# Optimization experiments

Measured on AMD Instinct MI355X. Metric: run time of the kernel, lower is better.

The kernel has to match this reference:

```python
import jax, jax.numpy as jnp
import numpy as np

H, W = 256, 832
B = 2
SEARCH_W, SEARCH_H = 7, 3
SPARSITY_RAD = 2
SENSE_RANGE = 10
PIX_W = 20.0          # pixel_distance_weight
ALPHA_W = 0.7         # alpha_distance_weight
MULLINE_W = 15.0      # pixel_mulline_distance_weight
ALPHA_PAD = 0.6       # alpha_padding
INF = 1e9


def _sorted_offsets(span_x, span_y):
    xs, ys = np.meshgrid(span_x, span_y)
    xs = xs.flatten(); ys = ys.flatten()
    order = np.argsort(xs ** 2 + ys ** 2, kind='stable')
    return xs[order].astype(np.int32), ys[order].astype(np.int32)


def setup_inputs() -> dict:
    key = jax.random.key(0)
    k1, k2 = jax.random.split(key)
    src = (jax.random.uniform(k1, (B, 1, H, W)) < 0.02).astype(jnp.float32)
    dst = (jax.random.uniform(k2, (B, 1, H, W)) < 0.02).astype(jnp.float32)
    xx, yy = _sorted_offsets(np.arange(-SEARCH_W, SEARCH_W + 1), np.arange(-SEARCH_H, SEARCH_H + 1))
    sxs, sys_ = np.meshgrid(np.arange(-SPARSITY_RAD, SPARSITY_RAD + 1), np.arange(-SPARSITY_RAD, SPARSITY_RAD + 1))
    sxx = sxs.flatten().astype(np.int32); syy = sys_.flatten().astype(np.int32)
    cxx, cyy = _sorted_offsets(np.arange(-SENSE_RANGE, SENSE_RANGE + 1), np.arange(-SENSE_RANGE, SENSE_RANGE + 1))
    return {"binMapsrc": src, "binMapdst": dst,
            "xx": jnp.asarray(xx), "yy": jnp.asarray(yy),
            "sxx": jnp.asarray(sxx), "syy": jnp.asarray(syy),
            "cxx": jnp.asarray(cxx), "cyy": jnp.asarray(cyy)}


def _orientation(m):
    # local edge orientation from a 3x3 box-blurred map
    b = sum(jnp.roll(jnp.roll(m, di, 0), dj, 1) for di in (-1, 0, 1) for dj in (-1, 0, 1))
    gy, gx = jnp.gradient(b)
    return jnp.arctan2(gy, gx)


def _morph_single(src, dst, xx, yy, sxx, syy, cxx, cyy):
    gy, gx = jnp.meshgrid(jnp.arange(H, dtype=jnp.int32), jnp.arange(W, dtype=jnp.int32), indexing='ij')

    def gather(offy, offx, arr, fill):
        ii = gy[None] + offy[:, None, None]          # [K,H,W]
        jj = gx[None] + offx[:, None, None]
        inb = (ii >= 0) & (ii < H) & (jj >= 0) & (jj < W)
        vals = arr[jnp.clip(ii, 0, H - 1), jnp.clip(jj, 0, W - 1)]
        return jnp.where(inb, vals, fill)

    src_e = src > 0.5
    # --- sparsify source edge points: keep min-linear-index edge in each sparsity window ---
    lin = jnp.where(src_e, (gy * W + gx).astype(jnp.float32), INF)
    keep = src_e & (lin == gather(syy, sxx, lin, INF).min(0))
    # --- windowed correspondence search with distance + orientation scoring ---
    theta_s = _orientation(src)
    theta_d = _orientation(dst)
    hit = gather(yy, xx, dst, 0.0) > 0.5             # [K,H,W]
    ang = 1.0 - jnp.cos(theta_s[None] - gather(yy, xx, theta_d, 0.0))
    dist = jnp.sqrt((xx * xx + yy * yy).astype(jnp.float32))
    score = jnp.where(hit, PIX_W * dist[:, None, None] + MULLINE_W * ALPHA_W * ang, INF)
    kbest = jnp.argmin(score, axis=0)                # [H,W]
    active = keep & (score.min(0) < 0.5 * INF)
    dispx = jnp.where(active, xx[kbest].astype(jnp.float32), 0.0)
    dispy = jnp.where(active, yy[kbest].astype(jnp.float32), 0.0)
    # --- diffuse sparse displacements over the sense window (scan keeps memory small) ---
    R = SENSE_RANGE
    pad = lambda a: jnp.pad(a, ((R, R), (R, R)))
    pdx, pdy, pm = pad(dispx), pad(dispy), pad(active.astype(jnp.float32))
    wk = jnp.exp(-jnp.sqrt((cxx * cxx + cyy * cyy).astype(jnp.float32)) / (0.5 * R))

    def body(carry, inp):
        nx, ny, den = carry
        dy_, dx_, w = inp
        sl = lambda a: jax.lax.dynamic_slice(a, (R + dy_, R + dx_), (H, W))
        return (nx + w * sl(pdx), ny + w * sl(pdy), den + w * sl(pm)), None

    zeros = jnp.zeros((H, W), jnp.float32)
    (nx, ny, den), _ = jax.lax.scan(body, (zeros, zeros, zeros), (cyy, cxx, wk))
    mdx = ALPHA_PAD * nx / (den + 1e-6)
    mdy = ALPHA_PAD * ny / (den + 1e-6)
    morphedx = gx.astype(jnp.float32) + mdx
    morphedy = gy.astype(jnp.float32) + mdy
    return jnp.stack([morphedx, morphedy], 0)        # [2,H,W]


def reference(binMapsrc, binMapdst, xx, yy, sxx, syy, cxx, cyy):
    f = lambda s, d: _morph_single(s, d, xx, yy, sxx, syy, cxx, cyy)
    return jax.vmap(f)(binMapsrc[:, 0], binMapdst[:, 0])  # [B,2,H,W]
```

## Files before the change

kernel.cpp:

```cpp
#include <hip/hip_runtime.h>
#include <math.h>

#define BB 2
#define HH 256
#define WW 832
#define HWIMG (HH * WW)
#define BHW (BB * HWIMG)

#define TXN 26
#define TYN 8
#define NTILES (BB * TXN * TYN)
#define CAP 512
#define LDSK 128

__device__ inline float theta_at(const float* __restrict__ m, int i, int j) {
    int ri[5], cj[5];
#pragma unroll
    for (int t = 0; t < 5; ++t) {
        int r = i + t - 2; r = (r < 0) ? r + HH : (r >= HH ? r - HH : r);
        int c = j + t - 2; c = (c < 0) ? c + WW : (c >= WW ? c - WW : c);
        ri[t] = r * WW; cj[t] = c;
    }
    float S[5][5];
#pragma unroll
    for (int a = 0; a < 5; ++a)
#pragma unroll
        for (int c = 0; c < 5; ++c)
            S[a][c] = m[ri[a] + cj[c]];
    float ct[5], cm[5], cb[5];
#pragma unroll
    for (int c = 0; c < 5; ++c) {
        ct[c] = S[0][c] + S[1][c] + S[2][c];
        cm[c] = S[1][c] + S[2][c] + S[3][c];
        cb[c] = S[2][c] + S[3][c] + S[4][c];
    }
    float Bm = ct[1] + ct[2] + ct[3];
    float Bp = cb[1] + cb[2] + cb[3];
    float Bl = cm[0] + cm[1] + cm[2];
    float Br = cm[2] + cm[3] + cm[4];
    float Bc = cm[1] + cm[2] + cm[3];
    float gy = (i == 0) ? (Bp - Bc) : (i == HH - 1) ? (Bc - Bm) : 0.5f * (Bp - Bm);
    float gx = (j == 0) ? (Br - Bc) : (j == WW - 1) ? (Bc - Bl) : 0.5f * (Br - Bl);
    return atan2f(gy, gx);
}

__global__ void fused_kernel(const float* __restrict__ src, const float* __restrict__ dst,
                             const int* __restrict__ xx, const int* __restrict__ yy, int K,
                             int* __restrict__ counts, int* __restrict__ entries) {
    __shared__ int kox[128], koy[128];
    __shared__ float kd[128];
    __shared__ int recs[LDSK];
    __shared__ float tss[LDSK];
    __shared__ int nkeep;

    int tid = threadIdx.x;
    if (tid == 0) nkeep = 0;
    for (int t = tid; t < K; t += 256) {
        int ox = xx[t], oy = yy[t];
        kox[t] = ox; koy[t] = oy;
        kd[t] = 20.0f * sqrtf((float)(ox * ox + oy * oy));
    }
    __syncthreads();

    int idx = blockIdx.x * 256 + tid;
    int j = idx % WW;
    int r = idx / WW;
    int i = r % HH;
    int b = r / HH;
    const float* sb = src + b * HWIMG;
    const float* db = dst + b * HWIMG;

    if (sb[i * WW + j] > 0.5f) {
        float m = 0.f;
#pragma unroll
        for (int p = 0; p < 12; ++p) {
            int di = (p < 5) ? -2 : (p < 10 ? -1 : 0);
            int dj = (p < 5) ? (p - 2) : (p < 10 ? (p - 7) : (p - 12));
            int ii = i + di, jj = j + dj;
            bool inb = (ii >= 0) && (jj >= 0) && (jj < WW);
            float v = sb[inb ? (ii * WW + jj) : 0];
            m = fmaxf(m, inb ? v : 0.f);
        }
        if (m <= 0.5f) {
            float ts = theta_at(sb, i, j);
            int pos = atomicAdd(&nkeep, 1);
            if (pos < LDSK) {
                recs[pos] = j | (i << 10) | (b << 18);
                tss[pos] = ts;
            }
        }
    }
    __syncthreads();

    int nk = (nkeep < LDSK) ? nkeep : LDSK;
    int lane = tid & 63;
    int wv = tid >> 6;
    for (int w = wv; w < nk; w += 4) {
        int rec = recs[w];
        float ts = tss[w];
        int kj = rec & 1023;
        int ki = (rec >> 10) & 255;
        int kb = rec >> 18;
        const float* d = dst + kb * HWIMG;

        float best = 1e9f;
        int bk = 1 << 20;
#pragma unroll
        for (int rr = 0; rr < 2; ++rr) {
            int k = lane + rr * 64;
            if (k < K) {
                int ii = ki + koy[k], jj = kj + kox[k];
                if (ii >= 0 && ii < HH && jj >= 0 && jj < WW && d[ii * WW + jj] > 0.5f) {
                    float td = theta_at(d, ii, jj);
                    float sc = kd[k] + 10.5f * (1.0f - cosf(ts - td));
                    if (sc < best || (sc == best && k < bk)) { best = sc; bk = k; }
                }
            }
        }
#pragma unroll
        for (int off = 32; off >= 1; off >>= 1) {
            float ob = __shfl_down(best, off, 64);
            int ok = __shfl_down(bk, off, 64);
            if (ob < best || (ob == best && ok < bk)) { best = ob; bk = ok; }
        }
        if (lane == 0 && best < 5e8f) {
            int dx = kox[bk], dy = koy[bk];
            int packed = kj | (ki << 10) | ((dx + 7) << 18) | ((dy + 3) << 22);
            int tx0 = max(kj - 10, 0) >> 5, tx1 = min(kj + 10, WW - 1) >> 5;
            int ty0 = max(ki - 10, 0) >> 5, ty1 = min(ki + 10, HH - 1) >> 5;
            for (int ty = ty0; ty <= ty1; ++ty)
                for (int tx = tx0; tx <= tx1; ++tx) {
                    int tile = (kb * TYN + ty) * TXN + tx;
                    int pos = atomicAdd(&counts[tile], 1);
                    if (pos < CAP) entries[tile * CAP + pos] = packed;
                }
        }
    }
}

__global__ void diffuse_kernel(const int* __restrict__ counts, const int* __restrict__ entries,
                               float* __restrict__ out) {
    __shared__ float wt[441];
    __shared__ float4 ent[CAP];
    int tid = threadIdx.y * 32 + threadIdx.x;
    for (int t = tid; t < 441; t += 256) {
        int dy = t / 21 - 10;
        int dx = t % 21 - 10;
        wt[t] = expf(-sqrtf((float)(dx * dx + dy * dy)) / 5.0f);
    }
    int tx = blockIdx.x, ty = blockIdx.y, b = blockIdx.z;
    int tile = (b * TYN + ty) * TXN + tx;
    int cnt = counts[tile];
    if (cnt > CAP) cnt = CAP;
    const int* e = entries + tile * CAP;
    for (int t = tid; t < cnt; t += 256) {
        int p = e[t];
        ent[t] = make_float4((float)(p & 1023), (float)((p >> 10) & 255),
                             (float)(((p >> 18) & 15) - 7), (float)(((p >> 22) & 7) - 3));
    }
    __syncthreads();

    int j = tx * 32 + threadIdx.x;
    int i0 = ty * 32 + threadIdx.y * 4;
    float nx0 = 0, ny0 = 0, de0 = 0;
    float nx1 = 0, ny1 = 0, de1 = 0;
    float nx2 = 0, ny2 = 0, de2 = 0;
    float nx3 = 0, ny3 = 0, de3 = 0;

    for (int c = 0; c < cnt; ++c) {
        float4 E = ent[c];
        int dj = (int)E.x - j;
        if (dj < -10 || dj > 10) continue;
        int di = (int)E.y - i0;
        const float* wrow = &wt[dj + 10];
        if (di >= -10 && di <= 10) { float w = wrow[(di + 10) * 21]; de0 += w; nx0 += w * E.z; ny0 += w * E.w; }
        if (di >= -9  && di <= 11) { float w = wrow[(di + 9)  * 21]; de1 += w; nx1 += w * E.z; ny1 += w * E.w; }
        if (di >= -8  && di <= 12) { float w = wrow[(di + 8)  * 21]; de2 += w; nx2 += w * E.z; ny2 += w * E.w; }
        if (di >= -7  && di <= 13) { float w = wrow[(di + 7)  * 21]; de3 += w; nx3 += w * E.z; ny3 += w * E.w; }
    }

    int obase = b * 2 * HWIMG;
    float inv;
    inv = 0.6f / (de0 + 1e-6f);
    out[obase + (i0 + 0) * WW + j] = (float)j + nx0 * inv;
    out[obase + HWIMG + (i0 + 0) * WW + j] = (float)(i0 + 0) + ny0 * inv;
    inv = 0.6f / (de1 + 1e-6f);
    out[obase + (i0 + 1) * WW + j] = (float)j + nx1 * inv;
    out[obase + HWIMG + (i0 + 1) * WW + j] = (float)(i0 + 1) + ny1 * inv;
    inv = 0.6f / (de2 + 1e-6f);
    out[obase + (i0 + 2) * WW + j] = (float)j + nx2 * inv;
    out[obase + HWIMG + (i0 + 2) * WW + j] = (float)(i0 + 2) + ny2 * inv;
    inv = 0.6f / (de3 + 1e-6f);
    out[obase + (i0 + 3) * WW + j] = (float)j + nx3 * inv;
    out[obase + HWIMG + (i0 + 3) * WW + j] = (float)(i0 + 3) + ny3 * inv;
}

extern "C" void kernel_launch(void* const* d_in, const int* in_sizes, int n_in,
                              void* d_out, int out_size, void* d_ws, size_t ws_size,
                              hipStream_t stream) {
    const float* src = (const float*)d_in[0];
    const float* dst = (const float*)d_in[1];
    const int* xx = (const int*)d_in[2];
    const int* yy = (const int*)d_in[3];
    int K = in_sizes[2];

    int* counts  = (int*)d_ws;
    int* entries = counts + NTILES;
    float* out = (float*)d_out;

    hipMemsetAsync(counts, 0, NTILES * sizeof(int), stream);
    fused_kernel<<<dim3(BHW / 256), dim3(256), 0, stream>>>(
        src, dst, xx, yy, K, counts, entries);
    diffuse_kernel<<<dim3(TXN, TYN, BB), dim3(32, 8), 0, stream>>>(counts, entries, out);
}
```

Baseline: 110.7 us.

## Merge edge selection, matching and diffusion into one cooperative kernel

Replaces the memset and the two kernel launches with a single cooperative kernel of 416 blocks that uses grid-wide syncs between phases. Tile counts are zeroed inside the kernel, and each thread now scans four source pixels loaded as a float4, so the block count matches the diffusion tile count. This is meant to remove launch and memset overhead. In exchange it pays for two grid barriers, cuts the parallelism of the scan phase by four, and adds per-block serial work over its retained edge points.

New measurement: 220.0 us. 98.7% more time.

```diff
diff --git a/kernel.cpp b/kernel.cpp
--- a/kernel.cpp
+++ b/kernel.cpp
@@ -1,5 +1,8 @@
 #include <hip/hip_runtime.h>
+#include <hip/hip_cooperative_groups.h>
 #include <math.h>
+
+namespace cg = cooperative_groups;
 
 #define BB 2
 #define HH 256
@@ -44,155 +47,170 @@
     return atan2f(gy, gx);
 }
 
-__global__ void fused_kernel(const float* __restrict__ src, const float* __restrict__ dst,
-                             const int* __restrict__ xx, const int* __restrict__ yy, int K,
-                             int* __restrict__ counts, int* __restrict__ entries) {
+__global__ void mega_kernel(const float4* __restrict__ src4, const float* __restrict__ src,
+                            const float* __restrict__ dst,
+                            const int* __restrict__ xx, const int* __restrict__ yy, int K,
+                            int* __restrict__ counts, int* __restrict__ entries,
+                            float* __restrict__ out) {
     __shared__ int kox[128], koy[128];
     __shared__ float kd[128];
     __shared__ int recs[LDSK];
     __shared__ float tss[LDSK];
     __shared__ int nkeep;
-
+    __shared__ float wt[441];
+    __shared__ float4 ent[CAP];
+
+    cg::grid_group grid = cg::this_grid();
     int tid = threadIdx.x;
-    if (tid == 0) nkeep = 0;
+    int bid = blockIdx.x;
+
+    if (tid == 0) { nkeep = 0; counts[bid] = 0; }
     for (int t = tid; t < K; t += 256) {
         int ox = xx[t], oy = yy[t];
         kox[t] = ox; koy[t] = oy;
         kd[t] = 20.0f * sqrtf((float)(ox * ox + oy * oy));
     }
-    __syncthreads();
-
-    int idx = blockIdx.x * 256 + tid;
-    int j = idx % WW;
-    int r = idx / WW;
-    int i = r % HH;
-    int b = r / HH;
-    const float* sb = src + b * HWIMG;
-    const float* db = dst + b * HWIMG;
-
-    if (sb[i * WW + j] > 0.5f) {
-        float m = 0.f;
-#pragma unroll
-        for (int p = 0; p < 12; ++p) {
-            int di = (p < 5) ? -2 : (p < 10 ? -1 : 0);
-            int dj = (p < 5) ? (p - 2) : (p < 10 ? (p - 7) : (p - 12));
-            int ii = i + di, jj = j + dj;
-            bool inb = (ii >= 0) && (jj >= 0) && (jj < WW);
-            float v = sb[inb ? (ii * WW + jj) : 0];
-            m = fmaxf(m, inb ? v : 0.f);
-        }
-        if (m <= 0.5f) {
-            float ts = theta_at(sb, i, j);
-            int pos = atomicAdd(&nkeep, 1);
-            if (pos < LDSK) {
-                recs[pos] = j | (i << 10) | (b << 18);
-                tss[pos] = ts;
-            }
-        }
-    }
-    __syncthreads();
-
-    int nk = (nkeep < LDSK) ? nkeep : LDSK;
-    int lane = tid & 63;
-    int wv = tid >> 6;
-    for (int w = wv; w < nk; w += 4) {
-        int rec = recs[w];
-        float ts = tss[w];
-        int kj = rec & 1023;
-        int ki = (rec >> 10) & 255;
-        int kb = rec >> 18;
-        const float* d = dst + kb * HWIMG;
-
-        float best = 1e9f;
-        int bk = 1 << 20;
-#pragma unroll
-        for (int rr = 0; rr < 2; ++rr) {
-            int k = lane + rr * 64;
-            if (k < K) {
-                int ii = ki + koy[k], jj = kj + kox[k];
-                if (ii >= 0 && ii < HH && jj >= 0 && jj < WW && d[ii * WW + jj] > 0.5f) {
-                    float td = theta_at(d, ii, jj);
-                    float sc = kd[k] + 10.5f * (1.0f - cosf(ts - td));
-                    if (sc < best || (sc == best && k < bk)) { best = sc; bk = k; }
-                }
-            }
-        }
-#pragma unroll
-        for (int off = 32; off >= 1; off >>= 1) {
-            float ob = __shfl_down(best, off, 64);
-            int ok = __shfl_down(bk, off, 64);
-            if (ob < best || (ob == best && ok < bk)) { best = ob; bk = ok; }
-        }
-        if (lane == 0 && best < 5e8f) {
-            int dx = kox[bk], dy = koy[bk];
-            int packed = kj | (ki << 10) | ((dx + 7) << 18) | ((dy + 3) << 22);
-            int tx0 = max(kj - 10, 0) >> 5, tx1 = min(kj + 10, WW - 1) >> 5;
-            int ty0 = max(ki - 10, 0) >> 5, ty1 = min(ki + 10, HH - 1) >> 5;
-            for (int ty = ty0; ty <= ty1; ++ty)
-                for (int tx = tx0; tx <= tx1; ++tx) {
-                    int tile = (kb * TYN + ty) * TXN + tx;
-                    int pos = atomicAdd(&counts[tile], 1);
-                    if (pos < CAP) entries[tile * CAP + pos] = packed;
-                }
-        }
-    }
-}
-
-__global__ void diffuse_kernel(const int* __restrict__ counts, const int* __restrict__ entries,
-                               float* __restrict__ out) {
-    __shared__ float wt[441];
-    __shared__ float4 ent[CAP];
-    int tid = threadIdx.y * 32 + threadIdx.x;
     for (int t = tid; t < 441; t += 256) {
         int dy = t / 21 - 10;
         int dx = t % 21 - 10;
         wt[t] = expf(-sqrtf((float)(dx * dx + dy * dy)) / 5.0f);
     }
-    int tx = blockIdx.x, ty = blockIdx.y, b = blockIdx.z;
-    int tile = (b * TYN + ty) * TXN + tx;
-    int cnt = counts[tile];
-    if (cnt > CAP) cnt = CAP;
-    const int* e = entries + tile * CAP;
-    for (int t = tid; t < cnt; t += 256) {
-        int p = e[t];
-        ent[t] = make_float4((float)(p & 1023), (float)((p >> 10) & 255),
-                             (float)(((p >> 18) & 15) - 7), (float)(((p >> 22) & 7) - 3));
-    }
     __syncthreads();
 
-    int j = tx * 32 + threadIdx.x;
-    int i0 = ty * 32 + threadIdx.y * 4;
-    float nx0 = 0, ny0 = 0, de0 = 0;
-    float nx1 = 0, ny1 = 0, de1 = 0;
-    float nx2 = 0, ny2 = 0, de2 = 0;
-    float nx3 = 0, ny3 = 0, de3 = 0;
-
-    for (int c = 0; c < cnt; ++c) {
-        float4 E = ent[c];
-        int dj = (int)E.x - j;
-        if (dj < -10 || dj > 10) continue;
-        int di = (int)E.y - i0;
-        const float* wrow = &wt[dj + 10];
-        if (di >= -10 && di <= 10) { float w = wrow[(di + 10) * 21]; de0 += w; nx0 += w * E.z; ny0 += w * E.w; }
-        if (di >= -9  && di <= 11) { float w = wrow[(di + 9)  * 21]; de1 += w; nx1 += w * E.z; ny1 += w * E.w; }
-        if (di >= -8  && di <= 12) { float w = wrow[(di + 8)  * 21]; de2 += w; nx2 += w * E.z; ny2 += w * E.w; }
-        if (di >= -7  && di <= 13) { float w = wrow[(di + 7)  * 21]; de3 += w; nx3 += w * E.z; ny3 += w * E.w; }
-    }
-
-    int obase = b * 2 * HWIMG;
-    float inv;
-    inv = 0.6f / (de0 + 1e-6f);
-    out[obase + (i0 + 0) * WW + j] = (float)j + nx0 * inv;
-    out[obase + HWIMG + (i0 + 0) * WW + j] = (float)(i0 + 0) + ny0 * inv;
-    inv = 0.6f / (de1 + 1e-6f);
-    out[obase + (i0 + 1) * WW + j] = (float)j + nx1 * inv;
-    out[obase + HWIMG + (i0 + 1) * WW + j] = (float)(i0 + 1) + ny1 * inv;
-    inv = 0.6f / (de2 + 1e-6f);
-    out[obase + (i0 + 2) * WW + j] = (float)j + nx2 * inv;
-    out[obase + HWIMG + (i0 + 2) * WW + j] = (float)(i0 + 2) + ny2 * inv;
-    inv = 0.6f / (de3 + 1e-6f);
-    out[obase + (i0 + 3) * WW + j] = (float)j + nx3 * inv;
-    out[obase + HWIMG + (i0 + 3) * WW + j] = (float)(i0 + 3) + ny3 * inv;
+    {
+        int t4 = bid * 256 + tid;
+        float4 sv = src4[t4];
+        int p0 = t4 * 4;
+        int j0 = p0 % WW;
+        int r = p0 / WW;
+        int i = r % HH;
+        int b = r / HH;
+        const float* sb = src + b * HWIMG;
+        float svv[4] = {sv.x, sv.y, sv.z, sv.w};
+#pragma unroll
+        for (int q = 0; q < 4; ++q) {
+            if (svv[q] > 0.5f) {
+                int j = j0 + q;
+                float m = 0.f;
+#pragma unroll
+                for (int p = 0; p < 12; ++p) {
+                    int di = (p < 5) ? -2 : (p < 10 ? -1 : 0);
+                    int dj = (p < 5) ? (p - 2) : (p < 10 ? (p - 7) : (p - 12));
+                    int ii = i + di, jj = j + dj;
+                    bool inb = (ii >= 0) && (jj >= 0) && (jj < WW);
+                    float v = sb[inb ? (ii * WW + jj) : 0];
+                    m = fmaxf(m, inb ? v : 0.f);
+                }
+                if (m <= 0.5f) {
+                    float ts = theta_at(sb, i, j);
+                    int pos = atomicAdd(&nkeep, 1);
+                    if (pos < LDSK) {
+                        recs[pos] = j | (i << 10) | (b << 18);
+                        tss[pos] = ts;
+                    }
+                }
+            }
+        }
+    }
+    grid.sync();
+
+    {
+        int nk = (nkeep < LDSK) ? nkeep : LDSK;
+        int lane = tid & 63;
+        int wv = tid >> 6;
+        for (int w = wv; w < nk; w += 4) {
+            int rec = recs[w];
+            float ts = tss[w];
+            int kj = rec & 1023;
+            int ki = (rec >> 10) & 255;
+            int kb = rec >> 18;
+            const float* d = dst + kb * HWIMG;
+
+            float best = 1e9f;
+            int bk = 1 << 20;
+#pragma unroll
+            for (int rr = 0; rr < 2; ++rr) {
+                int k = lane + rr * 64;
+                if (k < K) {
+                    int ii = ki + koy[k], jj = kj + kox[k];
+                    if (ii >= 0 && ii < HH && jj >= 0 && jj < WW && d[ii * WW + jj] > 0.5f) {
+                        float td = theta_at(d, ii, jj);
+                        float sc = kd[k] + 10.5f * (1.0f - cosf(ts - td));
+                        if (sc < best || (sc == best && k < bk)) { best = sc; bk = k; }
+                    }
+                }
+            }
+#pragma unroll
+            for (int off = 32; off >= 1; off >>= 1) {
+                float ob = __shfl_down(best, off, 64);
+                int ok = __shfl_down(bk, off, 64);
+                if (ob < best || (ob == best && ok < bk)) { best = ob; bk = ok; }
+            }
+            if (lane == 0 && best < 5e8f) {
+                int dx = kox[bk], dy = koy[bk];
+                int packed = kj | (ki << 10) | ((dx + 7) << 18) | ((dy + 3) << 22);
+                int tx0 = max(kj - 10, 0) >> 5, tx1 = min(kj + 10, WW - 1) >> 5;
+                int ty0 = max(ki - 10, 0) >> 5, ty1 = min(ki + 10, HH - 1) >> 5;
+                for (int ty = ty0; ty <= ty1; ++ty)
+                    for (int tx = tx0; tx <= tx1; ++tx) {
+                        int tile = (kb * TYN + ty) * TXN + tx;
+                        int pos = atomicAdd(&counts[tile], 1);
+                        if (pos < CAP) entries[tile * CAP + pos] = packed;
+                    }
+            }
+        }
+    }
+    grid.sync();
+
+    {
+        int b = bid / (TYN * TXN);
+        int rem = bid % (TYN * TXN);
+        int ty = rem / TXN;
+        int tx = rem % TXN;
+        int cnt = counts[bid];
+        if (cnt > CAP) cnt = CAP;
+        const int* e = entries + bid * CAP;
+        for (int t = tid; t < cnt; t += 256) {
+            int p = e[t];
+            ent[t] = make_float4((float)(p & 1023), (float)((p >> 10) & 255),
+                                 (float)(((p >> 18) & 15) - 7), (float)(((p >> 22) & 7) - 3));
+        }
+        __syncthreads();
+
+        int j = tx * 32 + (tid & 31);
+        int i0 = ty * 32 + (tid >> 5) * 4;
+        float nx0 = 0, ny0 = 0, de0 = 0;
+        float nx1 = 0, ny1 = 0, de1 = 0;
+        float nx2 = 0, ny2 = 0, de2 = 0;
+        float nx3 = 0, ny3 = 0, de3 = 0;
+
+        for (int c = 0; c < cnt; ++c) {
+            float4 E = ent[c];
+            int dj = (int)E.x - j;
+            if (dj < -10 || dj > 10) continue;
+            int di = (int)E.y - i0;
+            const float* wrow = &wt[dj + 10];
+            if (di >= -10 && di <= 10) { float w = wrow[(di + 10) * 21]; de0 += w; nx0 += w * E.z; ny0 += w * E.w; }
+            if (di >= -9  && di <= 11) { float w = wrow[(di + 9)  * 21]; de1 += w; nx1 += w * E.z; ny1 += w * E.w; }
+            if (di >= -8  && di <= 12) { float w = wrow[(di + 8)  * 21]; de2 += w; nx2 += w * E.z; ny2 += w * E.w; }
+            if (di >= -7  && di <= 13) { float w = wrow[(di + 7)  * 21]; de3 += w; nx3 += w * E.z; ny3 += w * E.w; }
+        }
+
+        int obase = b * 2 * HWIMG;
+        float inv;
+        inv = 0.6f / (de0 + 1e-6f);
+        out[obase + (i0 + 0) * WW + j] = (float)j + nx0 * inv;
+        out[obase + HWIMG + (i0 + 0) * WW + j] = (float)(i0 + 0) + ny0 * inv;
+        inv = 0.6f / (de1 + 1e-6f);
+        out[obase + (i0 + 1) * WW + j] = (float)j + nx1 * inv;
+        out[obase + HWIMG + (i0 + 1) * WW + j] = (float)(i0 + 1) + ny1 * inv;
+        inv = 0.6f / (de2 + 1e-6f);
+        out[obase + (i0 + 2) * WW + j] = (float)j + nx2 * inv;
+        out[obase + HWIMG + (i0 + 2) * WW + j] = (float)(i0 + 2) + ny2 * inv;
+        inv = 0.6f / (de3 + 1e-6f);
+        out[obase + (i0 + 3) * WW + j] = (float)j + nx3 * inv;
+        out[obase + HWIMG + (i0 + 3) * WW + j] = (float)(i0 + 3) + ny3 * inv;
+    }
 }
 
 extern "C" void kernel_launch(void* const* d_in, const int* in_sizes, int n_in,
@@ -207,9 +225,10 @@
     int* counts  = (int*)d_ws;
     int* entries = counts + NTILES;
     float* out = (float*)d_out;
-
-    hipMemsetAsync(counts, 0, NTILES * sizeof(int), stream);
-    fused_kernel<<<dim3(BHW / 256), dim3(256), 0, stream>>>(
-        src, dst, xx, yy, K, counts, entries);
-    diffuse_kernel<<<dim3(TXN, TYN, BB), dim3(32, 8), 0, stream>>>(counts, entries, out);
+    const float4* src4 = (const float4*)src;
+
+    void* args[] = {(void*)&src4, (void*)&src, (void*)&dst, (void*)&xx, (void*)&yy,
+                    (void*)&K, (void*)&counts, (void*)&entries, (void*)&out};
+    hipLaunchCooperativeKernel((void*)mega_kernel, dim3(NTILES), dim3(256),
+                               args, 0, stream);
 }
```

## Fuse keypoint detection, matching and diffusion into one tile kernel with LDS halos

Applied to the files above, without the earlier changes.

Replaces the memset, the global keypoint/matching kernel and the diffusion kernel with a single per-tile kernel. Each 32x32 tile loads halo windows of the src and dst maps into LDS. It recomputes the sparse source keypoints for its 52x52 neighbourhood, matches them against dst in LDS, and diffuses the results directly. This removes the global atomics, the entry buffer round trip and two launches, at the cost of redundant keypoint and matching work in overlapping halos and larger LDS use.

After: 117.2 us. 1.06x slower.

```diff
diff --git a/kernel.cpp b/kernel.cpp
--- a/kernel.cpp
+++ b/kernel.cpp
@@ -5,28 +5,24 @@
 #define HH 256
 #define WW 832
 #define HWIMG (HH * WW)
-#define BHW (BB * HWIMG)
 
 #define TXN 26
 #define TYN 8
-#define NTILES (BB * TXN * TYN)
-#define CAP 512
-#define LDSK 128
-
-__device__ inline float theta_at(const float* __restrict__ m, int i, int j) {
-    int ri[5], cj[5];
-#pragma unroll
-    for (int t = 0; t < 5; ++t) {
-        int r = i + t - 2; r = (r < 0) ? r + HH : (r >= HH ? r - HH : r);
-        int c = j + t - 2; c = (c < 0) ? c + WW : (c >= WW ? c - WW : c);
-        ri[t] = r * WW; cj[t] = c;
-    }
+#define CAP 256
+
+#define SH 56
+#define SW 56
+#define DH 62
+#define DW 70
+
+__device__ inline float theta_lds(const float* a, int pitch, int ly, int lx,
+                                  int gi, int gj) {
     float S[5][5];
 #pragma unroll
-    for (int a = 0; a < 5; ++a)
+    for (int r = 0; r < 5; ++r)
 #pragma unroll
         for (int c = 0; c < 5; ++c)
-            S[a][c] = m[ri[a] + cj[c]];
+            S[r][c] = a[(ly + r - 2) * pitch + (lx + c - 2)];
     float ct[5], cm[5], cb[5];
 #pragma unroll
     for (int c = 0; c < 5; ++c) {
@@ -39,160 +35,159 @@
     float Bl = cm[0] + cm[1] + cm[2];
     float Br = cm[2] + cm[3] + cm[4];
     float Bc = cm[1] + cm[2] + cm[3];
-    float gy = (i == 0) ? (Bp - Bc) : (i == HH - 1) ? (Bc - Bm) : 0.5f * (Bp - Bm);
-    float gx = (j == 0) ? (Br - Bc) : (j == WW - 1) ? (Bc - Bl) : 0.5f * (Br - Bl);
+    float gy = (gi == 0) ? (Bp - Bc) : (gi == HH - 1) ? (Bc - Bm) : 0.5f * (Bp - Bm);
+    float gx = (gj == 0) ? (Br - Bc) : (gj == WW - 1) ? (Bc - Bl) : 0.5f * (Br - Bl);
     return atan2f(gy, gx);
 }
 
-__global__ void fused_kernel(const float* __restrict__ src, const float* __restrict__ dst,
-                             const int* __restrict__ xx, const int* __restrict__ yy, int K,
-                             int* __restrict__ counts, int* __restrict__ entries) {
+__global__ void __launch_bounds__(256, 2)
+bnmorph_kernel(const float* __restrict__ src, const float* __restrict__ dst,
+               const int* __restrict__ xx, const int* __restrict__ yy, int K,
+               float* __restrict__ out) {
+    __shared__ float srcW[SH * SW];
+    __shared__ float dstW[DH * DW];
+    __shared__ float wt[441];
     __shared__ int kox[128], koy[128];
     __shared__ float kd[128];
-    __shared__ int recs[LDSK];
-    __shared__ float tss[LDSK];
+    __shared__ float4 ent[CAP];
     __shared__ int nkeep;
 
     int tid = threadIdx.x;
+    int tx = blockIdx.x, ty = blockIdx.y, b = blockIdx.z;
+    int ti = ty * 32, tj = tx * 32;
+    const float* sb = src + b * HWIMG;
+    const float* db = dst + b * HWIMG;
+
     if (tid == 0) nkeep = 0;
     for (int t = tid; t < K; t += 256) {
         int ox = xx[t], oy = yy[t];
         kox[t] = ox; koy[t] = oy;
         kd[t] = 20.0f * sqrtf((float)(ox * ox + oy * oy));
     }
-    __syncthreads();
-
-    int idx = blockIdx.x * 256 + tid;
-    int j = idx % WW;
-    int r = idx / WW;
-    int i = r % HH;
-    int b = r / HH;
-    const float* sb = src + b * HWIMG;
-    const float* db = dst + b * HWIMG;
-
-    if (sb[i * WW + j] > 0.5f) {
-        float m = 0.f;
-#pragma unroll
-        for (int p = 0; p < 12; ++p) {
-            int di = (p < 5) ? -2 : (p < 10 ? -1 : 0);
-            int dj = (p < 5) ? (p - 2) : (p < 10 ? (p - 7) : (p - 12));
-            int ii = i + di, jj = j + dj;
-            bool inb = (ii >= 0) && (jj >= 0) && (jj < WW);
-            float v = sb[inb ? (ii * WW + jj) : 0];
-            m = fmaxf(m, inb ? v : 0.f);
-        }
-        if (m <= 0.5f) {
-            float ts = theta_at(sb, i, j);
-            int pos = atomicAdd(&nkeep, 1);
-            if (pos < LDSK) {
-                recs[pos] = j | (i << 10) | (b << 18);
-                tss[pos] = ts;
-            }
-        }
-    }
-    __syncthreads();
-
-    int nk = (nkeep < LDSK) ? nkeep : LDSK;
-    int lane = tid & 63;
-    int wv = tid >> 6;
-    for (int w = wv; w < nk; w += 4) {
-        int rec = recs[w];
-        float ts = tss[w];
-        int kj = rec & 1023;
-        int ki = (rec >> 10) & 255;
-        int kb = rec >> 18;
-        const float* d = dst + kb * HWIMG;
-
-        float best = 1e9f;
-        int bk = 1 << 20;
-#pragma unroll
-        for (int rr = 0; rr < 2; ++rr) {
-            int k = lane + rr * 64;
-            if (k < K) {
-                int ii = ki + koy[k], jj = kj + kox[k];
-                if (ii >= 0 && ii < HH && jj >= 0 && jj < WW && d[ii * WW + jj] > 0.5f) {
-                    float td = theta_at(d, ii, jj);
-                    float sc = kd[k] + 10.5f * (1.0f - cosf(ts - td));
-                    if (sc < best || (sc == best && k < bk)) { best = sc; bk = k; }
-                }
-            }
-        }
-#pragma unroll
-        for (int off = 32; off >= 1; off >>= 1) {
-            float ob = __shfl_down(best, off, 64);
-            int ok = __shfl_down(bk, off, 64);
-            if (ob < best || (ob == best && ok < bk)) { best = ob; bk = ok; }
-        }
-        if (lane == 0 && best < 5e8f) {
-            int dx = kox[bk], dy = koy[bk];
-            int packed = kj | (ki << 10) | ((dx + 7) << 18) | ((dy + 3) << 22);
-            int tx0 = max(kj - 10, 0) >> 5, tx1 = min(kj + 10, WW - 1) >> 5;
-            int ty0 = max(ki - 10, 0) >> 5, ty1 = min(ki + 10, HH - 1) >> 5;
-            for (int ty = ty0; ty <= ty1; ++ty)
-                for (int tx = tx0; tx <= tx1; ++tx) {
-                    int tile = (kb * TYN + ty) * TXN + tx;
-                    int pos = atomicAdd(&counts[tile], 1);
-                    if (pos < CAP) entries[tile * CAP + pos] = packed;
-                }
-        }
-    }
-}
-
-__global__ void diffuse_kernel(const int* __restrict__ counts, const int* __restrict__ entries,
-                               float* __restrict__ out) {
-    __shared__ float wt[441];
-    __shared__ float4 ent[CAP];
-    int tid = threadIdx.y * 32 + threadIdx.x;
     for (int t = tid; t < 441; t += 256) {
         int dy = t / 21 - 10;
         int dx = t % 21 - 10;
         wt[t] = expf(-sqrtf((float)(dx * dx + dy * dy)) / 5.0f);
     }
-    int tx = blockIdx.x, ty = blockIdx.y, b = blockIdx.z;
-    int tile = (b * TYN + ty) * TXN + tx;
-    int cnt = counts[tile];
-    if (cnt > CAP) cnt = CAP;
-    const int* e = entries + tile * CAP;
-    for (int t = tid; t < cnt; t += 256) {
-        int p = e[t];
-        ent[t] = make_float4((float)(p & 1023), (float)((p >> 10) & 255),
-                             (float)(((p >> 18) & 15) - 7), (float)(((p >> 22) & 7) - 3));
+    const int SR0 = ti - 12, SC0 = tj - 12;
+    for (int t = tid; t < SH * SW; t += 256) {
+        int gi = SR0 + t / SW; gi = (gi + HH) % HH;
+        int gj = SC0 + t % SW; gj = (gj + WW) % WW;
+        srcW[t] = sb[gi * WW + gj];
+    }
+    const int DR0 = ti - 15, DC0 = tj - 19;
+    for (int t = tid; t < DH * DW; t += 256) {
+        int gi = DR0 + t / DW; gi = (gi + HH) % HH;
+        int gj = DC0 + t % DW; gj = (gj + WW) % WW;
+        dstW[t] = db[gi * WW + gj];
     }
     __syncthreads();
 
-    int j = tx * 32 + threadIdx.x;
-    int i0 = ty * 32 + threadIdx.y * 4;
-    float nx0 = 0, ny0 = 0, de0 = 0;
-    float nx1 = 0, ny1 = 0, de1 = 0;
-    float nx2 = 0, ny2 = 0, de2 = 0;
-    float nx3 = 0, ny3 = 0, de3 = 0;
-
-    for (int c = 0; c < cnt; ++c) {
-        float4 E = ent[c];
-        int dj = (int)E.x - j;
-        if (dj < -10 || dj > 10) continue;
-        int di = (int)E.y - i0;
-        const float* wrow = &wt[dj + 10];
-        if (di >= -10 && di <= 10) { float w = wrow[(di + 10) * 21]; de0 += w; nx0 += w * E.z; ny0 += w * E.w; }
-        if (di >= -9  && di <= 11) { float w = wrow[(di + 9)  * 21]; de1 += w; nx1 += w * E.z; ny1 += w * E.w; }
-        if (di >= -8  && di <= 12) { float w = wrow[(di + 8)  * 21]; de2 += w; nx2 += w * E.z; ny2 += w * E.w; }
-        if (di >= -7  && di <= 13) { float w = wrow[(di + 7)  * 21]; de3 += w; nx3 += w * E.z; ny3 += w * E.w; }
-    }
-
-    int obase = b * 2 * HWIMG;
-    float inv;
-    inv = 0.6f / (de0 + 1e-6f);
-    out[obase + (i0 + 0) * WW + j] = (float)j + nx0 * inv;
-    out[obase + HWIMG + (i0 + 0) * WW + j] = (float)(i0 + 0) + ny0 * inv;
-    inv = 0.6f / (de1 + 1e-6f);
-    out[obase + (i0 + 1) * WW + j] = (float)j + nx1 * inv;
-    out[obase + HWIMG + (i0 + 1) * WW + j] = (float)(i0 + 1) + ny1 * inv;
-    inv = 0.6f / (de2 + 1e-6f);
-    out[obase + (i0 + 2) * WW + j] = (float)j + nx2 * inv;
-    out[obase + HWIMG + (i0 + 2) * WW + j] = (float)(i0 + 2) + ny2 * inv;
-    inv = 0.6f / (de3 + 1e-6f);
-    out[obase + (i0 + 3) * WW + j] = (float)j + nx3 * inv;
-    out[obase + HWIMG + (i0 + 3) * WW + j] = (float)(i0 + 3) + ny3 * inv;
+    for (int t = tid; t < 52 * 52; t += 256) {
+        int ry = t / 52, rx = t % 52;
+        int gi = ti - 10 + ry;
+        int gj = tj - 10 + rx;
+        if (gi < 0 || gi >= HH || gj < 0 || gj >= WW) continue;
+        int sly = ry + 2, slx = rx + 2;
+        if (srcW[sly * SW + slx] > 0.5f) {
+            float m = 0.f;
+#pragma unroll
+            for (int p = 0; p < 12; ++p) {
+                int di = (p < 5) ? -2 : (p < 10 ? -1 : 0);
+                int dj = (p < 5) ? (p - 2) : (p < 10 ? (p - 7) : (p - 12));
+                int ii = gi + di, jj = gj + dj;
+                bool inb = (ii >= 0) && (jj >= 0) && (jj < WW);
+                float v = srcW[(sly + di) * SW + slx + dj];
+                m = fmaxf(m, inb ? v : 0.f);
+            }
+            if (m <= 0.5f) {
+                float ts = theta_lds(srcW, SW, sly, slx, gi, gj);
+                int pos = atomicAdd(&nkeep, 1);
+                if (pos < CAP) ent[pos] = make_float4((float)gj, (float)gi, ts, 0.f);
+            }
+        }
+    }
+    __syncthreads();
+
+    int nk = (nkeep < CAP) ? nkeep : CAP;
+    {
+        int lane = tid & 63;
+        int wv = tid >> 6;
+        for (int w = wv; w < nk; w += 4) {
+            float4 E = ent[w];
+            int gj = (int)E.x, gi = (int)E.y;
+            float ts = E.z;
+
+            float best = 1e9f;
+            int bk = 1 << 20;
+#pragma unroll
+            for (int rr = 0; rr < 2; ++rr) {
+                int k = lane + rr * 64;
+                if (k < K) {
+                    int pi = gi + koy[k], pj = gj + kox[k];
+                    if (pi >= 0 && pi < HH && pj >= 0 && pj < WW) {
+                        int dly = pi - DR0, dlx = pj - DC0;
+                        if (dstW[dly * DW + dlx] > 0.5f) {
+                            float td = theta_lds(dstW, DW, dly, dlx, pi, pj);
+                            float sc = kd[k] + 10.5f * (1.0f - cosf(ts - td));
+                            if (sc < best || (sc == best && k < bk)) { best = sc; bk = k; }
+                        }
+                    }
+                }
+            }
+#pragma unroll
+            for (int off = 32; off >= 1; off >>= 1) {
+                float ob = __shfl_down(best, off, 64);
+                int ok = __shfl_down(bk, off, 64);
+                if (ob < best || (ob == best && ok < bk)) { best = ob; bk = ok; }
+            }
+            if (lane == 0) {
+                if (best < 5e8f) {
+                    ent[w].z = (float)kox[bk];
+                    ent[w].w = (float)koy[bk];
+                } else {
+                    ent[w].x = -1e4f;
+                }
+            }
+        }
+    }
+    __syncthreads();
+
+    {
+        int j = tj + (tid & 31);
+        int i0 = ti + (tid >> 5) * 4;
+        float nx0 = 0, ny0 = 0, de0 = 0;
+        float nx1 = 0, ny1 = 0, de1 = 0;
+        float nx2 = 0, ny2 = 0, de2 = 0;
+        float nx3 = 0, ny3 = 0, de3 = 0;
+
+        for (int c = 0; c < nk; ++c) {
+            float4 E = ent[c];
+            int dj = (int)E.x - j;
+            if (dj < -10 || dj > 10) continue;
+            int di = (int)E.y - i0;
+            const float* wrow = &wt[dj + 10];
+            if (di >= -10 && di <= 10) { float w = wrow[(di + 10) * 21]; de0 += w; nx0 += w * E.z; ny0 += w * E.w; }
+            if (di >= -9  && di <= 11) { float w = wrow[(di + 9)  * 21]; de1 += w; nx1 += w * E.z; ny1 += w * E.w; }
+            if (di >= -8  && di <= 12) { float w = wrow[(di + 8)  * 21]; de2 += w; nx2 += w * E.z; ny2 += w * E.w; }
+            if (di >= -7  && di <= 13) { float w = wrow[(di + 7)  * 21]; de3 += w; nx3 += w * E.z; ny3 += w * E.w; }
+        }
+
+        int obase = b * 2 * HWIMG;
+        float inv;
+        inv = 0.6f / (de0 + 1e-6f);
+        out[obase + (i0 + 0) * WW + j] = (float)j + nx0 * inv;
+        out[obase + HWIMG + (i0 + 0) * WW + j] = (float)(i0 + 0) + ny0 * inv;
+        inv = 0.6f / (de1 + 1e-6f);
+        out[obase + (i0 + 1) * WW + j] = (float)j + nx1 * inv;
+        out[obase + HWIMG + (i0 + 1) * WW + j] = (float)(i0 + 1) + ny1 * inv;
+        inv = 0.6f / (de2 + 1e-6f);
+        out[obase + (i0 + 2) * WW + j] = (float)j + nx2 * inv;
+        out[obase + HWIMG + (i0 + 2) * WW + j] = (float)(i0 + 2) + ny2 * inv;
+        inv = 0.6f / (de3 + 1e-6f);
+        out[obase + (i0 + 3) * WW + j] = (float)j + nx3 * inv;
+        out[obase + HWIMG + (i0 + 3) * WW + j] = (float)(i0 + 3) + ny3 * inv;
+    }
 }
 
 extern "C" void kernel_launch(void* const* d_in, const int* in_sizes, int n_in,
@@ -204,12 +199,6 @@
     const int* yy = (const int*)d_in[3];
     int K = in_sizes[2];
 
-    int* counts  = (int*)d_ws;
-    int* entries = counts + NTILES;
-    float* out = (float*)d_out;
-
-    hipMemsetAsync(counts, 0, NTILES * sizeof(int), stream);
-    fused_kernel<<<dim3(BHW / 256), dim3(256), 0, stream>>>(
-        src, dst, xx, yy, K, counts, entries);
-    diffuse_kernel<<<dim3(TXN, TYN, BB), dim3(32, 8), 0, stream>>>(counts, entries, out);
+    bnmorph_kernel<<<dim3(TXN, TYN, BB), dim3(256), 0, stream>>>(
+        src, dst, xx, yy, K, (float*)d_out);
 }
```

## Replace atomic tile scatter with per-tile segments gathered from 3x3 neighbors

Applied to the files above, without the earlier changes.

The search kernel now runs on 16x16 2D tiles and writes each tile's kept edge points and their displacements into a fixed per-tile segment, with no global atomics. The diffuse kernel gathers entries from the 3x3 neighboring segments into shared memory, and each thread computes one output pixel. This removes the memset, the global atomic scatter into overlapping 32x32 tiles, and the 4-row register blocking. In exchange, each diffuse tile scans up to 9 segments, and the fixed caps (64 per tile, 192 per neighborhood) could drop entries on dense inputs.

Measured after the change: 91.78 us (median of 2 runs). -17.1%, faster.

```diff
diff --git a/kernel.cpp b/kernel.cpp
--- a/kernel.cpp
+++ b/kernel.cpp
@@ -5,13 +5,11 @@
 #define HH 256
 #define WW 832
 #define HWIMG (HH * WW)
-#define BHW (BB * HWIMG)
-
-#define TXN 26
-#define TYN 8
-#define NTILES (BB * TXN * TYN)
-#define CAP 512
-#define LDSK 128
+
+#define TX2 52
+#define TY2 16
+#define SEG 64
+#define ECAP 192
 
 __device__ inline float theta_at(const float* __restrict__ m, int i, int j) {
     int ri[5], cj[5];
@@ -44,13 +42,14 @@
     return atan2f(gy, gx);
 }
 
-__global__ void fused_kernel(const float* __restrict__ src, const float* __restrict__ dst,
-                             const int* __restrict__ xx, const int* __restrict__ yy, int K,
-                             int* __restrict__ counts, int* __restrict__ entries) {
+__global__ void prep_search_kernel(const float* __restrict__ src, const float* __restrict__ dst,
+                                   const int* __restrict__ xx, const int* __restrict__ yy, int K,
+                                   int* __restrict__ cnt, int* __restrict__ seg) {
     __shared__ int kox[128], koy[128];
     __shared__ float kd[128];
-    __shared__ int recs[LDSK];
-    __shared__ float tss[LDSK];
+    __shared__ int recs[SEG];
+    __shared__ float tss[SEG];
+    __shared__ int outv[SEG];
     __shared__ int nkeep;
 
     int tid = threadIdx.x;
@@ -62,46 +61,39 @@
     }
     __syncthreads();
 
-    int idx = blockIdx.x * 256 + tid;
-    int j = idx % WW;
-    int r = idx / WW;
-    int i = r % HH;
-    int b = r / HH;
+    int txi = blockIdx.x, tyi = blockIdx.y, b = blockIdx.z;
+    int gi = tyi * 16 + (tid >> 4);
+    int gj = txi * 16 + (tid & 15);
     const float* sb = src + b * HWIMG;
     const float* db = dst + b * HWIMG;
 
-    if (sb[i * WW + j] > 0.5f) {
+    if (sb[gi * WW + gj] > 0.5f) {
         float m = 0.f;
 #pragma unroll
         for (int p = 0; p < 12; ++p) {
             int di = (p < 5) ? -2 : (p < 10 ? -1 : 0);
             int dj = (p < 5) ? (p - 2) : (p < 10 ? (p - 7) : (p - 12));
-            int ii = i + di, jj = j + dj;
+            int ii = gi + di, jj = gj + dj;
             bool inb = (ii >= 0) && (jj >= 0) && (jj < WW);
             float v = sb[inb ? (ii * WW + jj) : 0];
             m = fmaxf(m, inb ? v : 0.f);
         }
         if (m <= 0.5f) {
-            float ts = theta_at(sb, i, j);
+            float ts = theta_at(sb, gi, gj);
             int pos = atomicAdd(&nkeep, 1);
-            if (pos < LDSK) {
-                recs[pos] = j | (i << 10) | (b << 18);
-                tss[pos] = ts;
-            }
-        }
-    }
-    __syncthreads();
-
-    int nk = (nkeep < LDSK) ? nkeep : LDSK;
+            if (pos < SEG) { recs[pos] = gj | (gi << 10); tss[pos] = ts; }
+        }
+    }
+    __syncthreads();
+
+    int nk = (nkeep < SEG) ? nkeep : SEG;
     int lane = tid & 63;
     int wv = tid >> 6;
     for (int w = wv; w < nk; w += 4) {
         int rec = recs[w];
+        int kj = rec & 1023;
+        int ki = rec >> 10;
         float ts = tss[w];
-        int kj = rec & 1023;
-        int ki = (rec >> 10) & 255;
-        int kb = rec >> 18;
-        const float* d = dst + kb * HWIMG;
 
         float best = 1e9f;
         int bk = 1 << 20;
@@ -109,9 +101,9 @@
         for (int rr = 0; rr < 2; ++rr) {
             int k = lane + rr * 64;
             if (k < K) {
-                int ii = ki + koy[k], jj = kj + kox[k];
-                if (ii >= 0 && ii < HH && jj >= 0 && jj < WW && d[ii * WW + jj] > 0.5f) {
-                    float td = theta_at(d, ii, jj);
+                int pi = ki + koy[k], pj = kj + kox[k];
+                if (pi >= 0 && pi < HH && pj >= 0 && pj < WW && db[pi * WW + pj] > 0.5f) {
+                    float td = theta_at(db, pi, pj);
                     float sc = kd[k] + 10.5f * (1.0f - cosf(ts - td));
                     if (sc < best || (sc == best && k < bk)) { best = sc; bk = k; }
                 }
@@ -123,76 +115,75 @@
             int ok = __shfl_down(bk, off, 64);
             if (ob < best || (ob == best && ok < bk)) { best = ob; bk = ok; }
         }
-        if (lane == 0 && best < 5e8f) {
-            int dx = kox[bk], dy = koy[bk];
-            int packed = kj | (ki << 10) | ((dx + 7) << 18) | ((dy + 3) << 22);
-            int tx0 = max(kj - 10, 0) >> 5, tx1 = min(kj + 10, WW - 1) >> 5;
-            int ty0 = max(ki - 10, 0) >> 5, ty1 = min(ki + 10, HH - 1) >> 5;
-            for (int ty = ty0; ty <= ty1; ++ty)
-                for (int tx = tx0; tx <= tx1; ++tx) {
-                    int tile = (kb * TYN + ty) * TXN + tx;
-                    int pos = atomicAdd(&counts[tile], 1);
-                    if (pos < CAP) entries[tile * CAP + pos] = packed;
-                }
-        }
-    }
-}
-
-__global__ void diffuse_kernel(const int* __restrict__ counts, const int* __restrict__ entries,
+        if (lane == 0)
+            outv[w] = (best < 5e8f)
+                ? (rec | (b << 18) | ((kox[bk] + 7) << 19) | ((koy[bk] + 3) << 23))
+                : -1;
+    }
+    __syncthreads();
+
+    int tile = (b * TY2 + tyi) * TX2 + txi;
+    if (tid < nk) seg[tile * SEG + tid] = outv[tid];
+    if (tid == 0) cnt[tile] = nk;
+}
+
+__global__ void diffuse_kernel(const int* __restrict__ cnt, const int* __restrict__ seg,
                                float* __restrict__ out) {
     __shared__ float wt[441];
-    __shared__ float4 ent[CAP];
-    int tid = threadIdx.y * 32 + threadIdx.x;
+    __shared__ float4 ent[ECAP];
+    __shared__ int ncnt[9];
+    __shared__ int ne;
+
+    int tid = threadIdx.x;
+    if (tid == 0) ne = 0;
     for (int t = tid; t < 441; t += 256) {
         int dy = t / 21 - 10;
         int dx = t % 21 - 10;
         wt[t] = expf(-sqrtf((float)(dx * dx + dy * dy)) / 5.0f);
     }
-    int tx = blockIdx.x, ty = blockIdx.y, b = blockIdx.z;
-    int tile = (b * TYN + ty) * TXN + tx;
-    int cnt = counts[tile];
-    if (cnt > CAP) cnt = CAP;
-    const int* e = entries + tile * CAP;
-    for (int t = tid; t < cnt; t += 256) {
-        int p = e[t];
-        ent[t] = make_float4((float)(p & 1023), (float)((p >> 10) & 255),
-                             (float)(((p >> 18) & 15) - 7), (float)(((p >> 22) & 7) - 3));
-    }
-    __syncthreads();
-
-    int j = tx * 32 + threadIdx.x;
-    int i0 = ty * 32 + threadIdx.y * 4;
-    float nx0 = 0, ny0 = 0, de0 = 0;
-    float nx1 = 0, ny1 = 0, de1 = 0;
-    float nx2 = 0, ny2 = 0, de2 = 0;
-    float nx3 = 0, ny3 = 0, de3 = 0;
-
-    for (int c = 0; c < cnt; ++c) {
+    int txi = blockIdx.x, tyi = blockIdx.y, b = blockIdx.z;
+    if (tid < 9) {
+        int nty = tyi + tid / 3 - 1;
+        int ntx = txi + tid % 3 - 1;
+        ncnt[tid] = (nty >= 0 && nty < TY2 && ntx >= 0 && ntx < TX2)
+                        ? cnt[(b * TY2 + nty) * TX2 + ntx] : 0;
+    }
+    __syncthreads();
+
+    for (int t = tid; t < 9 * SEG; t += 256) {
+        int q = t / SEG, slot = t % SEG;
+        if (slot < ncnt[q]) {
+            int nty = tyi + q / 3 - 1;
+            int ntx = txi + q % 3 - 1;
+            int v = seg[((b * TY2 + nty) * TX2 + ntx) * SEG + slot];
+            if (v != -1) {
+                int pos = atomicAdd(&ne, 1);
+                if (pos < ECAP)
+                    ent[pos] = make_float4((float)(v & 1023), (float)((v >> 10) & 255),
+                                           (float)(((v >> 19) & 15) - 7),
+                                           (float)(((v >> 23) & 7) - 3));
+            }
+        }
+    }
+    __syncthreads();
+
+    int nn = (ne < ECAP) ? ne : ECAP;
+    int gj = txi * 16 + (tid & 15);
+    int gi = tyi * 16 + (tid >> 4);
+    float nx = 0.f, ny = 0.f, de = 0.f;
+    for (int c = 0; c < nn; ++c) {
         float4 E = ent[c];
-        int dj = (int)E.x - j;
-        if (dj < -10 || dj > 10) continue;
-        int di = (int)E.y - i0;
-        const float* wrow = &wt[dj + 10];
-        if (di >= -10 && di <= 10) { float w = wrow[(di + 10) * 21]; de0 += w; nx0 += w * E.z; ny0 += w * E.w; }
-        if (di >= -9  && di <= 11) { float w = wrow[(di + 9)  * 21]; de1 += w; nx1 += w * E.z; ny1 += w * E.w; }
-        if (di >= -8  && di <= 12) { float w = wrow[(di + 8)  * 21]; de2 += w; nx2 += w * E.z; ny2 += w * E.w; }
-        if (di >= -7  && di <= 13) { float w = wrow[(di + 7)  * 21]; de3 += w; nx3 += w * E.z; ny3 += w * E.w; }
-    }
-
+        int dj = (int)E.x - gj;
+        int di = (int)E.y - gi;
+        if (dj >= -10 && dj <= 10 && di >= -10 && di <= 10) {
+            float w = wt[(di + 10) * 21 + dj + 10];
+            de += w; nx += w * E.z; ny += w * E.w;
+        }
+    }
+    float inv = 0.6f / (de + 1e-6f);
     int obase = b * 2 * HWIMG;
-    float inv;
-    inv = 0.6f / (de0 + 1e-6f);
-    out[obase + (i0 + 0) * WW + j] = (float)j + nx0 * inv;
-    out[obase + HWIMG + (i0 + 0) * WW + j] = (float)(i0 + 0) + ny0 * inv;
-    inv = 0.6f / (de1 + 1e-6f);
-    out[obase + (i0 + 1) * WW + j] = (float)j + nx1 * inv;
-    out[obase + HWIMG + (i0 + 1) * WW + j] = (float)(i0 + 1) + ny1 * inv;
-    inv = 0.6f / (de2 + 1e-6f);
-    out[obase + (i0 + 2) * WW + j] = (float)j + nx2 * inv;
-    out[obase + HWIMG + (i0 + 2) * WW + j] = (float)(i0 + 2) + ny2 * inv;
-    inv = 0.6f / (de3 + 1e-6f);
-    out[obase + (i0 + 3) * WW + j] = (float)j + nx3 * inv;
-    out[obase + HWIMG + (i0 + 3) * WW + j] = (float)(i0 + 3) + ny3 * inv;
+    out[obase + gi * WW + gj] = (float)gj + nx * inv;
+    out[obase + HWIMG + gi * WW + gj] = (float)gi + ny * inv;
 }
 
 extern "C" void kernel_launch(void* const* d_in, const int* in_sizes, int n_in,
@@ -204,12 +195,11 @@
     const int* yy = (const int*)d_in[3];
     int K = in_sizes[2];
 
-    int* counts  = (int*)d_ws;
-    int* entries = counts + NTILES;
+    int* cnt = (int*)d_ws;
+    int* seg = cnt + BB * TY2 * TX2;
     float* out = (float*)d_out;
 
-    hipMemsetAsync(counts, 0, NTILES * sizeof(int), stream);
-    fused_kernel<<<dim3(BHW / 256), dim3(256), 0, stream>>>(
-        src, dst, xx, yy, K, counts, entries);
-    diffuse_kernel<<<dim3(TXN, TYN, BB), dim3(32, 8), 0, stream>>>(counts, entries, out);
-}
+    dim3 grid(TX2, TY2, BB);
+    prep_search_kernel<<<grid, dim3(256), 0, stream>>>(src, dst, xx, yy, K, cnt, seg);
+    diffuse_kernel<<<grid, dim3(256), 0, stream>>>(cnt, seg, out);
+}
```
